# Optimization experiments

Measured on AMD Instinct MI355X. Metric: run time of the kernel, lower is better.

The kernel has to match this reference:

```python
import jax, jax.numpy as jnp
import numpy as np


def setup_inputs() -> dict:
    key = jax.random.key(0)
    k1, k2, k3, k4 = jax.random.split(key, 4)
    B, S, D = 8, 2048, 512
    scale = 1.0 / np.sqrt(D)
    return {
        "x": jax.random.normal(k1, (B, S, D), dtype=jnp.float32),
        "WQ": jax.random.normal(k2, (D, D), dtype=jnp.float32) * scale,
        "WK": jax.random.normal(k3, (D, D), dtype=jnp.float32) * scale,
        "WV": jax.random.normal(k4, (D, D), dtype=jnp.float32) * scale,
    }


def reference(x, WQ, WK, WV):
    # x: [B, S, D]; single-head scaled dot-product self-attention
    Q = jnp.einsum("bsd,de->bse", x, WQ)
    K = jnp.einsum("bsd,de->bse", x, WK)
    V = jnp.einsum("bsd,de->bse", x, WV)
    d_k = jnp.asarray(K.shape[-1], dtype=x.dtype)
    scores = jnp.einsum("bqd,bkd->bqk", Q, K) / jnp.sqrt(d_k)  # [B,S,S]
    weights = jax.nn.softmax(scores, axis=-1)
    return jnp.einsum("bqk,bkd->bqd", weights, V)
```

## Files before the change

### kernel.cpp

```cpp
#include <hip/hip_runtime.h>
#include <cstdint>
#include <cstddef>

#define B_ 8
#define S_ 2048
#define D_ 512

typedef float f32x4 __attribute__((ext_vector_type(4)));
typedef __bf16 bf16x8 __attribute__((ext_vector_type(8)));

__device__ __forceinline__ unsigned short f2bf(float f) {
    unsigned u = __builtin_bit_cast(unsigned, f);
    u += 0x7FFFu + ((u >> 16) & 1u);
    return (unsigned short)(u >> 16);
}

__device__ __forceinline__ void gll16(const void* g, void* l) {
    __builtin_amdgcn_global_load_lds(
        (const __attribute__((address_space(1))) unsigned int*)g,
        (__attribute__((address_space(3))) unsigned int*)l, 16, 0, 0);
}

#define VMCNT(n) asm volatile("s_waitcnt vmcnt(%0)" :: "i"(n) : "memory")
#define LGKM0()  asm volatile("s_waitcnt lgkmcnt(0)" ::: "memory")
#define SBAR()   __builtin_amdgcn_s_barrier()
#define SCHED0() __builtin_amdgcn_sched_barrier(0)

template<int AMT, int BNT>
__global__ __launch_bounds__(512, 2) void gemm8(
    const unsigned short* __restrict__ A,
    const unsigned short* __restrict__ B,
    void* __restrict__ Cv,
    unsigned short* __restrict__ Cv2,
    int K, int lda, int ldb, int ldc, int ntn)
{
    constexpr int BM     = 64 * AMT;
    constexpr int BN     = 128 * BNT;
    constexpr int ABYTES = BM * 128;
    constexpr int BBYTES = BN * 128;
    constexpr int AH     = ABYTES / 2;
    constexpr int BH     = BBYTES / 2;
    constexpr int AGL    = AMT / 2;
    constexpr int BGL    = BNT;
    constexpr int BUFB   = ABYTES + BBYTES;
    __shared__ __align__(16) char lds[2 * BUFB];

    const int tq  = blockIdx.x;
    const int tn  = tq % ntn;
    const int tm  = tq / ntn;
    const int m0   = tm * BM;
    const int n0   = tn * BN;
    const int tid  = threadIdx.x;
    const int lane = tid & 63;
    const int w    = tid >> 6;
    const int g2   = w >> 2;
    const int nb   = w & 3;

    const int lrow = lane >> 3;
    const int swz  = ((lane & 7) ^ lrow) << 3;
    const unsigned short* gA[2][AGL];
    const unsigned short* gB[2][BGL];
    #pragma unroll
    for (int h = 0; h < 2; ++h) {
        #pragma unroll
        for (int i = 0; i < AGL; ++i)
            gA[h][i] = A + (size_t)(m0 + h * (BM / 2) + (w * AGL + i) * 8 + lrow) * lda + swz;
        #pragma unroll
        for (int i = 0; i < BGL; ++i)
            gB[h][i] = B + (size_t)(n0 + h * (BN / 2) + (w * BGL + i) * 8 + lrow) * ldb + swz;
    }
    auto stA = [&](int bs, int h, int kof) {
        #pragma unroll
        for (int i = 0; i < AGL; ++i)
            gll16(gA[h][i] + kof, lds + bs * BUFB + h * AH + (w * AGL + i) * 1024);
    };
    auto stB = [&](int bs, int h, int kof) {
        #pragma unroll
        for (int i = 0; i < BGL; ++i)
            gll16(gB[h][i] + kof, lds + bs * BUFB + ABYTES + h * BH + (w * BGL + i) * 1024);
    };

    const int fr = lane & 15;
    const int gq = lane >> 4;
    const int c0 = (gq ^ (fr & 7)) << 4;
    int aoff[AMT], boff[BNT];
    #pragma unroll
    for (int ml = 0; ml < AMT; ++ml)
        aoff[ml] = (g2 * (16 * AMT) + ml * 16 + fr) * 128 + c0;
    #pragma unroll
    for (int nl = 0; nl < BNT; ++nl)
        boff[nl] = (nb * (16 * BNT) + nl * 16 + fr) * 128 + c0;

    bf16x8 af[2 * AMT], bLO[2 * BNT], bHI[2 * BNT];
    f32x4 acc[2 * AMT][2 * BNT] = {};

    auto ldA = [&](const char* Ab, int mh) {
        #pragma unroll
        for (int ml = 0; ml < AMT; ++ml)
            #pragma unroll
            for (int kk = 0; kk < 2; ++kk)
                af[ml * 2 + kk] = *(const bf16x8*)(Ab + mh * AH + (aoff[ml] ^ (kk << 6)));
    };
    auto ldB = [&](const char* Bb, int nh, bf16x8* bf) {
        #pragma unroll
        for (int nl = 0; nl < BNT; ++nl)
            #pragma unroll
            for (int kk = 0; kk < 2; ++kk)
                bf[nl * 2 + kk] = *(const bf16x8*)(Bb + nh * BH + (boff[nl] ^ (kk << 6)));
    };
    auto mma = [&](int mh, int nh, const bf16x8* bf) {
        __builtin_amdgcn_s_setprio(1);
        #pragma unroll
        for (int ml = 0; ml < AMT; ++ml)
            #pragma unroll
            for (int nl = 0; nl < BNT; ++nl)
                #pragma unroll
                for (int kk = 0; kk < 2; ++kk)
                    acc[mh * AMT + ml][nh * BNT + nl] =
                        __builtin_amdgcn_mfma_f32_16x16x32_bf16(
                            af[ml * 2 + kk], bf[nl * 2 + kk],
                            acc[mh * AMT + ml][nh * BNT + nl], 0, 0, 0);
        __builtin_amdgcn_s_setprio(0);
    };

    stA(0, 0, 0);  stB(0, 0, 0);
    stA(0, 1, 0);  stB(0, 1, 0);
    stA(1, 0, 64); stB(1, 0, 64);

    const int NT = K >> 6;
    for (int tt = 0; tt < NT; ++tt) {
        const int bs = tt & 1;
        const char* Ab = lds + bs * BUFB;
        const char* Bb = Ab + ABYTES;
        const bool last = (tt == NT - 1);

        if (!last) stA(bs ^ 1, 1, (tt + 1) << 6);
        if (last) { VMCNT(AGL + BGL); } else { VMCNT(6); }
        SBAR(); SCHED0();
        ldA(Ab, 0); ldB(Bb, 0, bLO);
        mma(0, 0, bLO);

        if (!last) stB(bs ^ 1, 1, (tt + 1) << 6);
        if (last) { VMCNT(0); } else { VMCNT(6); }
        SBAR(); SCHED0();
        ldB(Bb, 1, bHI);
        mma(0, 1, bHI);

        if (tt + 2 < NT) stA(bs, 0, (tt + 2) << 6);
        VMCNT(6);
        SBAR(); SCHED0();
        ldA(Ab, 1);
        mma(1, 0, bLO);

        if (tt + 2 < NT) stB(bs, 0, (tt + 2) << 6);
        VMCNT(6);
        SBAR(); SCHED0();
        mma(1, 1, bHI);
    }

    const int rb4 = gq << 2;
#define AB_(mt) ((((mt) / AMT) * (BM / 2)) + g2 * (16 * AMT) + ((mt) % AMT) * 16)
#define BB_(nt) ((((nt) / BNT) * (BN / 2)) + nb * (16 * BNT) + ((nt) % BNT) * 16)
    if (tn >= 4) {
        #pragma unroll
        for (int mt = 0; mt < 2 * AMT; ++mt) {
            const int s0q = m0 + AB_(mt) + rb4;
            const int b   = s0q >> 11;
            const int se  = s0q & (S_ - 1);
            #pragma unroll
            for (int nt = 0; nt < 2 * BNT; ++nt) {
                const int d = (n0 - 2 * D_) + BB_(nt) + fr;
                ushort4 u;
                u.x = f2bf(acc[mt][nt][0]);
                u.y = f2bf(acc[mt][nt][1]);
                u.z = f2bf(acc[mt][nt][2]);
                u.w = f2bf(acc[mt][nt][3]);
                *(ushort4*)&Cv2[((size_t)b * D_ + d) * S_ + se] = u;
            }
        }
    } else {
        unsigned short* C = (unsigned short*)Cv;
        #pragma unroll
        for (int mt = 0; mt < 2 * AMT; ++mt)
            #pragma unroll
            for (int nt = 0; nt < 2 * BNT; ++nt) {
                const int gc = n0 + BB_(nt) + fr;
                #pragma unroll
                for (int r = 0; r < 4; ++r)
                    C[(size_t)(m0 + AB_(mt) + rb4 + r) * ldc + gc] = f2bf(acc[mt][nt][r]);
            }
    }
#undef AB_
#undef BB_
}

__global__ __launch_bounds__(512, 2) void fused_attn(
    const unsigned short* __restrict__ qk,
    const unsigned short* __restrict__ vtb,
    float* __restrict__ out,
    float scale)
{
    __shared__ __align__(16) char lds[148480];
    char* const QL = lds;
    char* const KV = lds + 65536;
    char* const PB = lds + 131072;
    float* const RS = (float*)(lds + 147456);

    const int lin = blockIdx.x;
    const int bz  = lin & 7;
    const int q0  = (lin >> 3) * 64;
    const int tid = threadIdx.x;
    const int lane = tid & 63;
    const int w   = tid >> 6;
    const int fr  = lane & 15;
    const int gq  = lane >> 4;
    const int g4  = w >> 1;
    const int qh  = w & 1;
    const int k7  = fr & 7;

    int row4[4], sc4[4];
    #pragma unroll
    for (int i = 0; i < 4; ++i) {
        const int off = tid * 16 + i * 8192;
        row4[i] = off >> 8;
        sc4[i]  = ((((off >> 4) & 15) ^ (row4[i] & 7)) << 3);
    }
    const size_t qrowb = (size_t)bz * S_;

    auto stK = [&](int b, int kv0, int j) {
        #pragma unroll
        for (int i = 0; i < 4; ++i)
            gll16(qk + (qrowb + kv0 + row4[i]) * 1024 + 512 + j * 128 + sc4[i],
                  KV + b * 32768 + tid * 16 + i * 8192);
    };
    auto stV = [&](int b, int kv0, int c) {
        #pragma unroll
        for (int i = 0; i < 4; ++i)
            gll16(vtb + ((size_t)bz * D_ + c * 128 + row4[i]) * S_ + kv0 + sc4[i],
                  KV + b * 32768 + tid * 16 + i * 8192);
    };
    auto stQall = [&]() {
        #pragma unroll
        for (int i = 0; i < 8; ++i) {
            const int off = tid * 16 + i * 8192;
            const int row = off >> 10;
            const int cl  = (off >> 4) & 63;
            const int cp  = (cl & 56) | ((cl & 7) ^ (row & 7));
            gll16(qk + (qrowb + q0 + row) * 1024 + cp * 8, QL + off);
        }
    };

    f32x4 acc_pv[4][4] = {};
    float rs0 = 0.f, rs1 = 0.f;

    stQall(); stK(0, 0, 0);
    int cur = 0;

    for (int kvi = 0; kvi < 16; ++kvi) {
        const int kv0 = kvi * 128;
        f32x4 acc_s[2][2] = {};

        #pragma unroll
        for (int j = 0; j < 4; ++j) {
            VMCNT(0);
            SBAR(); SCHED0();
            if (j < 3) stK(cur ^ 1, kv0, j + 1);
            else       stV(cur ^ 1, kv0, 0);
            const char* Kb = KV + cur * 32768;
            __builtin_amdgcn_s_setprio(1);
            #pragma unroll
            for (int kk = 0; kk < 4; ++kk) {
                const int ch = ((kk * 4 + gq) ^ k7) << 4;
                const bf16x8 kf0 = *(const bf16x8*)(Kb + (g4 * 32 + fr) * 256 + ch);
                const bf16x8 kf1 = *(const bf16x8*)(Kb + (g4 * 32 + 16 + fr) * 256 + ch);
                const int cl = j * 16 + kk * 4 + gq;
                const int cp = ((cl & 56) | ((cl & 7) ^ k7)) << 4;
                const bf16x8 qf0 = *(const bf16x8*)(QL + (qh * 32 + fr) * 1024 + cp);
                const bf16x8 qf1 = *(const bf16x8*)(QL + (qh * 32 + 16 + fr) * 1024 + cp);
                acc_s[0][0] = __builtin_amdgcn_mfma_f32_16x16x32_bf16(kf0, qf0, acc_s[0][0], 0, 0, 0);
                acc_s[0][1] = __builtin_amdgcn_mfma_f32_16x16x32_bf16(kf0, qf1, acc_s[0][1], 0, 0, 0);
                acc_s[1][0] = __builtin_amdgcn_mfma_f32_16x16x32_bf16(kf1, qf0, acc_s[1][0], 0, 0, 0);
                acc_s[1][1] = __builtin_amdgcn_mfma_f32_16x16x32_bf16(kf1, qf1, acc_s[1][1], 0, 0, 0);
            }
            __builtin_amdgcn_s_setprio(0);
            cur ^= 1;
        }

        #pragma unroll
        for (int mt = 0; mt < 2; ++mt)
            #pragma unroll
            for (int qf = 0; qf < 2; ++qf) {
                float p0 = __expf(acc_s[mt][qf][0] * scale);
                float p1 = __expf(acc_s[mt][qf][1] * scale);
                float p2 = __expf(acc_s[mt][qf][2] * scale);
                float p3 = __expf(acc_s[mt][qf][3] * scale);
                if (qf == 0) rs0 += (p0 + p1) + (p2 + p3);
                else         rs1 += (p0 + p1) + (p2 + p3);
                ushort4 u;
                u.x = f2bf(p0); u.y = f2bf(p1); u.z = f2bf(p2); u.w = f2bf(p3);
                const int row   = qh * 32 + qf * 16 + fr;
                const int chunk = g4 * 4 + mt * 2 + (gq >> 1);
                *(ushort4*)(PB + row * 256 + ((chunk ^ k7) << 4) + (gq & 1) * 8) = u;
            }
        VMCNT(0);
        LGKM0();
        SBAR(); SCHED0();

        bf16x8 pf[4][4];
        #pragma unroll
        for (int nt2 = 0; nt2 < 4; ++nt2)
            #pragma unroll
            for (int ks = 0; ks < 4; ++ks)
                pf[nt2][ks] = *(const bf16x8*)(
                    PB + (nt2 * 16 + fr) * 256 + (((ks * 4 + gq) ^ k7) << 4));

        #pragma unroll
        for (int c = 0; c < 4; ++c) {
            if (c > 0) { VMCNT(0); SBAR(); SCHED0(); }
            if (c < 3)          stV(cur ^ 1, kv0, c + 1);
            else if (kvi < 15)  stK(cur ^ 1, kv0 + 128, 0);
            const char* Vb = KV + cur * 32768;
            __builtin_amdgcn_s_setprio(1);
            #pragma unroll
            for (int ks = 0; ks < 4; ++ks) {
                const bf16x8 vf = *(const bf16x8*)(
                    Vb + (w * 16 + fr) * 256 + (((ks * 4 + gq) ^ k7) << 4));
                #pragma unroll
                for (int nt2 = 0; nt2 < 4; ++nt2)
                    acc_pv[c][nt2] = __builtin_amdgcn_mfma_f32_16x16x32_bf16(
                        vf, pf[nt2][ks], acc_pv[c][nt2], 0, 0, 0);
            }
            __builtin_amdgcn_s_setprio(0);
            cur ^= 1;
        }
    }

    rs0 += __shfl_xor(rs0, 16); rs0 += __shfl_xor(rs0, 32);
    rs1 += __shfl_xor(rs1, 16); rs1 += __shfl_xor(rs1, 32);
    if (lane < 16) {
        RS[g4 * 64 + qh * 32 + lane]      = rs0;
        RS[g4 * 64 + qh * 32 + 16 + lane] = rs1;
    }
    __syncthreads();

    #pragma unroll
    for (int nt2 = 0; nt2 < 4; ++nt2) {
        const int q = nt2 * 16 + fr;
        const float inv = __builtin_amdgcn_rcpf(
            (RS[q] + RS[64 + q]) + (RS[128 + q] + RS[192 + q]));
        float* op = out + ((qrowb + q0 + q) * D_);
        #pragma unroll
        for (int c = 0; c < 4; ++c) {
            const int d0 = c * 128 + w * 16 + gq * 4;
            float4 o;
            o.x = acc_pv[c][nt2][0] * inv;
            o.y = acc_pv[c][nt2][1] * inv;
            o.z = acc_pv[c][nt2][2] * inv;
            o.w = acc_pv[c][nt2][3] * inv;
            *(float4*)(op + d0) = o;
        }
    }
}

__global__ __launch_bounds__(256) void convert_x4(const float* __restrict__ x,
                                                  unsigned short* __restrict__ xb) {
    const size_t i = ((size_t)blockIdx.x * 256 + threadIdx.x) * 4;
    const float4 f = *(const float4*)(x + i);
    ushort4 u;
    u.x = f2bf(f.x); u.y = f2bf(f.y); u.z = f2bf(f.z); u.w = f2bf(f.w);
    *(ushort4*)(xb + i) = u;
}

__global__ __launch_bounds__(256) void convert_w(const float* __restrict__ WQ,
                                                 const float* __restrict__ WK,
                                                 const float* __restrict__ WV,
                                                 unsigned short* __restrict__ WT) {
    const int o = blockIdx.x * 256 + threadIdx.x;
    const float* W = blockIdx.y == 0 ? WQ : (blockIdx.y == 1 ? WK : WV);
    const int e = o >> 9, d = o & (D_ - 1);
    WT[(size_t)blockIdx.y * D_ * D_ + o] = f2bf(W[d * D_ + e]);
}

extern "C" void kernel_launch(void* const* d_in, const int* in_sizes, int n_in,
                              void* d_out, int out_size, void* d_ws, size_t ws_size,
                              hipStream_t stream)
{
    const float* x  = (const float*)d_in[0];
    const float* WQ = (const float*)d_in[1];
    const float* WK = (const float*)d_in[2];
    const float* WV = (const float*)d_in[3];

    unsigned short* ws  = (unsigned short*)d_ws;
    const size_t NX = (size_t)B_ * S_ * D_;
    unsigned short* xb  = ws;
    unsigned short* wtb = xb + NX;
    unsigned short* qk  = wtb + 3 * D_ * D_;
    unsigned short* vtb = qk + NX * 2;

    convert_x4<<<dim3((unsigned)(NX / 4 / 256)), 256, 0, stream>>>(x, xb);
    convert_w<<<dim3(D_ * D_ / 256, 3), 256, 0, stream>>>(WQ, WK, WV, wtb);

    gemm8<4, 2><<<dim3(384), 512, 0, stream>>>(
        xb, wtb, qk, vtb, D_, D_, D_, 2 * D_,  6);

    fused_attn<<<dim3(256), 512, 0, stream>>>(
        qk, vtb, (float*)d_out, 0.04419417382415922f);
}
```

Before: 230.6 us.

## Hold Q fragments in registers and use four-slot K/V ring buffer

After: 309.4 us. 1.34x slower.

```diff
diff --git a/kernel.cpp b/kernel.cpp
--- a/kernel.cpp
+++ b/kernel.cpp
@@ -201,10 +201,9 @@
     float scale)
 {
     __shared__ __align__(16) char lds[148480];
-    char* const QL = lds;
-    char* const KV = lds + 65536;
-    char* const PB = lds + 131072;
-    float* const RS = (float*)(lds + 147456);
+    char* const RING = lds;
+    char* const PB   = lds + 131072;
+    float* const RS  = (float*)(lds + 147456);
 
     const int lin = blockIdx.x;
     const int bz  = lin & 7;
@@ -227,34 +226,33 @@
     }
     const size_t qrowb = (size_t)bz * S_;
 
-    auto stK = [&](int b, int kv0, int j) {
+    auto stK = [&](int slot, int kv0, int j) {
         #pragma unroll
         for (int i = 0; i < 4; ++i)
             gll16(qk + (qrowb + kv0 + row4[i]) * 1024 + 512 + j * 128 + sc4[i],
-                  KV + b * 32768 + tid * 16 + i * 8192);
-    };
-    auto stV = [&](int b, int kv0, int c) {
+                  RING + slot * 32768 + tid * 16 + i * 8192);
+    };
+    auto stV = [&](int slot, int kv0, int c) {
         #pragma unroll
         for (int i = 0; i < 4; ++i)
             gll16(vtb + ((size_t)bz * D_ + c * 128 + row4[i]) * S_ + kv0 + sc4[i],
-                  KV + b * 32768 + tid * 16 + i * 8192);
-    };
-    auto stQall = [&]() {
-        #pragma unroll
-        for (int i = 0; i < 8; ++i) {
-            const int off = tid * 16 + i * 8192;
-            const int row = off >> 10;
-            const int cl  = (off >> 4) & 63;
-            const int cp  = (cl & 56) | ((cl & 7) ^ (row & 7));
-            gll16(qk + (qrowb + q0 + row) * 1024 + cp * 8, QL + off);
-        }
-    };
+                  RING + slot * 32768 + tid * 16 + i * 8192);
+    };
+
+    bf16x8 qreg[2][16];
+    #pragma unroll
+    for (int qf = 0; qf < 2; ++qf)
+        #pragma unroll
+        for (int c = 0; c < 16; ++c)
+            qreg[qf][c] = *(const bf16x8*)(
+                qk + (qrowb + q0 + qh * 32 + qf * 16 + fr) * 1024 + c * 32 + gq * 8);
+    SCHED0();
 
     f32x4 acc_pv[4][4] = {};
     float rs0 = 0.f, rs1 = 0.f;
 
-    stQall(); stK(0, 0, 0);
-    int cur = 0;
+    stK(0, 0, 0); stK(1, 0, 1);
+    SCHED0();
 
     for (int kvi = 0; kvi < 16; ++kvi) {
         const int kv0 = kvi * 128;
@@ -262,28 +260,30 @@
 
         #pragma unroll
         for (int j = 0; j < 4; ++j) {
-            VMCNT(0);
+            if (j < 2) { VMCNT(4); } else { VMCNT(8); }
             SBAR(); SCHED0();
-            if (j < 3) stK(cur ^ 1, kv0, j + 1);
-            else       stV(cur ^ 1, kv0, 0);
-            const char* Kb = KV + cur * 32768;
+            if      (j == 0) stK(2, kv0, 2);
+            else if (j == 1) { stK(3, kv0, 3); stV(0, kv0, 0); }
+            else if (j == 2) stV(1, kv0, 1);
+            else             stV(2, kv0, 2);
+            SCHED0();
+            const char* Kb = RING + j * 32768;
             __builtin_amdgcn_s_setprio(1);
             #pragma unroll
             for (int kk = 0; kk < 4; ++kk) {
                 const int ch = ((kk * 4 + gq) ^ k7) << 4;
                 const bf16x8 kf0 = *(const bf16x8*)(Kb + (g4 * 32 + fr) * 256 + ch);
                 const bf16x8 kf1 = *(const bf16x8*)(Kb + (g4 * 32 + 16 + fr) * 256 + ch);
-                const int cl = j * 16 + kk * 4 + gq;
-                const int cp = ((cl & 56) | ((cl & 7) ^ k7)) << 4;
-                const bf16x8 qf0 = *(const bf16x8*)(QL + (qh * 32 + fr) * 1024 + cp);
-                const bf16x8 qf1 = *(const bf16x8*)(QL + (qh * 32 + 16 + fr) * 1024 + cp);
-                acc_s[0][0] = __builtin_amdgcn_mfma_f32_16x16x32_bf16(kf0, qf0, acc_s[0][0], 0, 0, 0);
-                acc_s[0][1] = __builtin_amdgcn_mfma_f32_16x16x32_bf16(kf0, qf1, acc_s[0][1], 0, 0, 0);
-                acc_s[1][0] = __builtin_amdgcn_mfma_f32_16x16x32_bf16(kf1, qf0, acc_s[1][0], 0, 0, 0);
-                acc_s[1][1] = __builtin_amdgcn_mfma_f32_16x16x32_bf16(kf1, qf1, acc_s[1][1], 0, 0, 0);
+                acc_s[0][0] = __builtin_amdgcn_mfma_f32_16x16x32_bf16(
+                    kf0, qreg[0][j * 4 + kk], acc_s[0][0], 0, 0, 0);
+                acc_s[0][1] = __builtin_amdgcn_mfma_f32_16x16x32_bf16(
+                    kf0, qreg[1][j * 4 + kk], acc_s[0][1], 0, 0, 0);
+                acc_s[1][0] = __builtin_amdgcn_mfma_f32_16x16x32_bf16(
+                    kf1, qreg[0][j * 4 + kk], acc_s[1][0], 0, 0, 0);
+                acc_s[1][1] = __builtin_amdgcn_mfma_f32_16x16x32_bf16(
+                    kf1, qreg[1][j * 4 + kk], acc_s[1][1], 0, 0, 0);
             }
             __builtin_amdgcn_s_setprio(0);
-            cur ^= 1;
         }
 
         #pragma unroll
@@ -302,37 +302,48 @@
                 const int chunk = g4 * 4 + mt * 2 + (gq >> 1);
                 *(ushort4*)(PB + row * 256 + ((chunk ^ k7) << 4) + (gq & 1) * 8) = u;
             }
+        LGKM0();
+        VMCNT(4);
+        SBAR(); SCHED0();
+        stV(3, kv0, 3);
+        SCHED0();
+        __builtin_amdgcn_s_setprio(1);
+        #pragma unroll
+        for (int ks = 0; ks < 4; ++ks) {
+            const int ch = ((ks * 4 + gq) ^ k7) << 4;
+            const bf16x8 vf0 = *(const bf16x8*)(RING + (w * 16 + fr) * 256 + ch);
+            const bf16x8 vf1 = *(const bf16x8*)(RING + 32768 + (w * 16 + fr) * 256 + ch);
+            #pragma unroll
+            for (int nt2 = 0; nt2 < 4; ++nt2) {
+                const bf16x8 pf = *(const bf16x8*)(PB + (nt2 * 16 + fr) * 256 + ch);
+                acc_pv[0][nt2] = __builtin_amdgcn_mfma_f32_16x16x32_bf16(
+                    vf0, pf, acc_pv[0][nt2], 0, 0, 0);
+                acc_pv[1][nt2] = __builtin_amdgcn_mfma_f32_16x16x32_bf16(
+                    vf1, pf, acc_pv[1][nt2], 0, 0, 0);
+            }
+        }
+        __builtin_amdgcn_s_setprio(0);
+
         VMCNT(0);
-        LGKM0();
-        SBAR(); SCHED0();
-
-        bf16x8 pf[4][4];
-        #pragma unroll
-        for (int nt2 = 0; nt2 < 4; ++nt2)
-            #pragma unroll
-            for (int ks = 0; ks < 4; ++ks)
-                pf[nt2][ks] = *(const bf16x8*)(
-                    PB + (nt2 * 16 + fr) * 256 + (((ks * 4 + gq) ^ k7) << 4));
-
-        #pragma unroll
-        for (int c = 0; c < 4; ++c) {
-            if (c > 0) { VMCNT(0); SBAR(); SCHED0(); }
-            if (c < 3)          stV(cur ^ 1, kv0, c + 1);
-            else if (kvi < 15)  stK(cur ^ 1, kv0 + 128, 0);
-            const char* Vb = KV + cur * 32768;
-            __builtin_amdgcn_s_setprio(1);
-            #pragma unroll
-            for (int ks = 0; ks < 4; ++ks) {
-                const bf16x8 vf = *(const bf16x8*)(
-                    Vb + (w * 16 + fr) * 256 + (((ks * 4 + gq) ^ k7) << 4));
-                #pragma unroll
-                for (int nt2 = 0; nt2 < 4; ++nt2)
-                    acc_pv[c][nt2] = __builtin_amdgcn_mfma_f32_16x16x32_bf16(
-                        vf, pf[nt2][ks], acc_pv[c][nt2], 0, 0, 0);
-            }
-            __builtin_amdgcn_s_setprio(0);
-            cur ^= 1;
+        SBAR(); SCHED0();
+        if (kvi < 15) { stK(0, kv0 + 128, 0); stK(1, kv0 + 128, 1); }
+        SCHED0();
+        __builtin_amdgcn_s_setprio(1);
+        #pragma unroll
+        for (int ks = 0; ks < 4; ++ks) {
+            const int ch = ((ks * 4 + gq) ^ k7) << 4;
+            const bf16x8 vf2 = *(const bf16x8*)(RING + 65536 + (w * 16 + fr) * 256 + ch);
+            const bf16x8 vf3 = *(const bf16x8*)(RING + 98304 + (w * 16 + fr) * 256 + ch);
+            #pragma unroll
+            for (int nt2 = 0; nt2 < 4; ++nt2) {
+                const bf16x8 pf = *(const bf16x8*)(PB + (nt2 * 16 + fr) * 256 + ch);
+                acc_pv[2][nt2] = __builtin_amdgcn_mfma_f32_16x16x32_bf16(
+                    vf2, pf, acc_pv[2][nt2], 0, 0, 0);
+                acc_pv[3][nt2] = __builtin_amdgcn_mfma_f32_16x16x32_bf16(
+                    vf3, pf, acc_pv[3][nt2], 0, 0, 0);
+            }
         }
+        __builtin_amdgcn_s_setprio(0);
     }
 
     rs0 += __shfl_xor(rs0, 16); rs0 += __shfl_xor(rs0, 32);
```
